# Performance work log

Measured on AMD Instinct MI355X. Metric: run time of the kernel, lower is better.

Reference implementation:

```python
import jax, jax.numpy as jnp
import numpy as np


def setup_inputs() -> dict:
    key = jax.random.key(0)
    ks = jax.random.split(key, 5)
    n, raw, d, h = 1024, 128, 128, 256
    s = lambda fan: 1.0 / np.sqrt(fan)
    return {
        "x": jax.random.normal(ks[0], (n, raw), jnp.float32),
        "W_enc": jax.random.normal(ks[1], (raw, d), jnp.float32) * s(raw),
        "b_enc": jnp.zeros((d,), jnp.float32),
        "W1": jax.random.normal(ks[2], (2 * d, h), jnp.float32) * s(2 * d),
        "b1": jnp.zeros((h,), jnp.float32),
        "W2": jax.random.normal(ks[3], (h, 1), jnp.float32) * s(h),
        "b2": jnp.zeros((1,), jnp.float32),
    }


def reference(x, W_enc, b_enc, W1, b1, W2, b2):
    # pathVAE.encode stand-in: linear projection to latent mean
    z = x @ W_enc + b_enc                      # [n, d]
    n, d = z.shape
    # Original builds feat[i, j] = concat(z[j], z[i]) of shape [n*n, 2d],
    # then Linear(2d->h). Split W1 so the quadratic concat is never built:
    # h[i, j] = z[j] @ W1[:d] + z[i] @ W1[d:] + b1
    A = z @ W1[:d]                             # acts on the "a" (j) half
    B = z @ W1[d:]                             # acts on the "b" (i) half
    hmat = A[None, :, :] + B[:, None, :] + b1  # [n, n, h]
    hmat = jax.nn.selu(hmat)
    o = hmat @ W2 + b2                         # [n, n, 1]
    o = jax.nn.hard_sigmoid(o)                 # relu6(x+3)/6, same as torch
    return o.reshape(n, n)
```

## Files before the change

kernel.cpp:

```cpp
#include <hip/hip_runtime.h>
#include <math.h>


#define LOG2E       1.4426950408889634f
#define SELU_AS     1.7580993408473766f
#define S_OVER_L2E  0.7282921587620419f

typedef float v2f __attribute__((ext_vector_type(2)));
typedef _Float16 v2h __attribute__((ext_vector_type(2)));
typedef unsigned int u32;

__global__ __launch_bounds__(256) void prep_kernel(
    const float* __restrict__ x, const float* __restrict__ W_enc,
    const float* __restrict__ b_enc, const float* __restrict__ W1,
    const float* __restrict__ b1, const float* __restrict__ W2,
    const float* __restrict__ b2, u32* __restrict__ PAa,
    u32* __restrict__ PAe, u32* __restrict__ PBb, u32* __restrict__ PBe,
    u32* __restrict__ W2m, u32* __restrict__ W2e, float* __restrict__ basep)
{
    __shared__ float zs[512];
    int t = threadIdx.x, b = blockIdx.x;
    if (b < 256) {
        int r0 = b << 2;
        int r = t >> 6;
        int dd = (t & 63) << 1;
        const float* xr = x + (size_t)(r0 + r) * 128;
        v2f z = { b_enc[dd], b_enc[dd + 1] };
#pragma unroll 8
        for (int dl = 0; dl < 128; ++dl) {
            float xv = xr[dl];
            v2f xx = { xv, xv };
            v2f wv = *(const v2f*)(W_enc + (size_t)dl * 128 + dd);
            z = __builtin_elementwise_fma(xx, wv, z);
        }
        zs[r * 128 + dd] = z.x;
        zs[r * 128 + dd + 1] = z.y;
        __syncthreads();

        int c = t;
        float b1c = b1[c];
        float accA0 = 0.f, accA1 = 0.f, accA2 = 0.f, accA3 = 0.f;
        float accB0 = b1c, accB1 = b1c, accB2 = b1c, accB3 = b1c;
        const float* w1a = W1 + c;
        const float* w1b = W1 + 128 * 256 + c;
#pragma unroll 4
        for (int dl = 0; dl < 128; ++dl) {
            float wa = w1a[(size_t)dl * 256];
            float wb = w1b[(size_t)dl * 256];
            float z0 = zs[dl], z1 = zs[128 + dl], z2 = zs[256 + dl], z3 = zs[384 + dl];
            accA0 = fmaf(z0, wa, accA0); accB0 = fmaf(z0, wb, accB0);
            accA1 = fmaf(z1, wa, accA1); accB1 = fmaf(z1, wb, accB1);
            accA2 = fmaf(z2, wa, accA2); accB2 = fmaf(z2, wb, accB2);
            accA3 = fmaf(z3, wa, accA3); accB3 = fmaf(z3, wb, accB3);
        }
        float ar[4] = { accA0 * LOG2E, accA1 * LOG2E, accA2 * LOG2E, accA3 * LOG2E };
        float br[4] = { accB0 * LOG2E, accB1 * LOG2E, accB2 * LOG2E, accB3 * LOG2E };
        u32 pa[4], pe[4], pb[4], pf[4];
        bool odd = (c & 1);
#pragma unroll
        for (int r2 = 0; r2 < 4; ++r2) {
            float er = __builtin_amdgcn_exp2f(ar[r2]);
            float fr = __builtin_amdgcn_exp2f(br[r2]);
            float aN = __shfl_xor(ar[r2], 1);
            float eN = __shfl_xor(er, 1);
            float bN = __shfl_xor(br[r2], 1);
            float fN = __shfl_xor(fr, 1);
            pa[r2] = __builtin_bit_cast(u32, __builtin_amdgcn_cvt_pkrtz(ar[r2], aN));
            pe[r2] = __builtin_bit_cast(u32, __builtin_amdgcn_cvt_pkrtz(er, eN));
            pb[r2] = __builtin_bit_cast(u32, __builtin_amdgcn_cvt_pkrtz(bN, br[r2]));
            pf[r2] = __builtin_bit_cast(u32, __builtin_amdgcn_cvt_pkrtz(fN, fr));
        }
        size_t o = (size_t)(c >> 1) * 1024 + r0;
        if (!odd) {
            *(uint4*)(PAa + o) = make_uint4(pa[0], pa[1], pa[2], pa[3]);
            *(uint4*)(PAe + o) = make_uint4(pe[0], pe[1], pe[2], pe[3]);
        } else {
            *(uint4*)(PBb + o) = make_uint4(pb[0], pb[1], pb[2], pb[3]);
            *(uint4*)(PBe + o) = make_uint4(pf[0], pf[1], pf[2], pf[3]);
        }
    } else {
        if (t < 128) {
            float w0 = W2[2 * t], w1 = W2[2 * t + 1];
            W2m[t] = __builtin_bit_cast(u32,
                __builtin_amdgcn_cvt_pkrtz(S_OVER_L2E * w0, S_OVER_L2E * w1));
            W2e[t] = __builtin_bit_cast(u32,
                __builtin_amdgcn_cvt_pkrtz(SELU_AS * w0, SELU_AS * w1));
        }
        if (t < 64) {
            float s = W2[t] + W2[t + 64] + W2[t + 128] + W2[t + 192];
#pragma unroll
            for (int o = 32; o > 0; o >>= 1) s += __shfl_down(s, o);
            if (t == 0) basep[0] = fmaf(-SELU_AS, s, b2[0]);
        }
    }
}

__global__ __launch_bounds__(256, 4) void pair_kernel(
    const u32* __restrict__ PAa, const u32* __restrict__ PAe,
    const u32* __restrict__ PBb, const u32* __restrict__ PBe,
    const u32* __restrict__ W2m, const u32* __restrict__ W2e,
    float* __restrict__ P)
{
    __shared__ __align__(16) u32 Aa[32 * 64];
    __shared__ __align__(16) u32 Ae[32 * 64];
    __shared__ __align__(16) u32 Bb[32 * 64];
    __shared__ __align__(16) u32 Be[32 * 64];

    int t = threadIdx.x;
    int bj64 = blockIdx.x << 6, bi64 = blockIdx.y << 6;
    int kc = blockIdx.z;
    int tj4 = (t & 15) << 2, ti4 = (t >> 4) << 2;

    float acc[4][4];
#pragma unroll
    for (int i = 0; i < 4; ++i)
#pragma unroll
        for (int j = 0; j < 4; ++j) acc[i][j] = 0.f;

    const v2h hzero = { (_Float16)0.f, (_Float16)0.f };
    const v2h hone  = { (_Float16)1.f, (_Float16)1.f };

#pragma unroll
    for (int p = 0; p < 2; ++p) {
        int q = (p << 8) + t;
        int k2l = q >> 4;
        int jq = (q & 15) << 2;
        size_t go = (size_t)((kc << 5) + k2l) * 1024;
        *(uint4*)&Aa[q << 2] = *(const uint4*)(PAa + go + bj64 + jq);
        *(uint4*)&Ae[q << 2] = *(const uint4*)(PAe + go + bj64 + jq);
        *(uint4*)&Bb[q << 2] = *(const uint4*)(PBb + go + bi64 + jq);
        *(uint4*)&Be[q << 2] = *(const uint4*)(PBe + go + bi64 + jq);
    }
    __syncthreads();

    const u32* Wm = W2m + (kc << 5);
    const u32* We = W2e + (kc << 5);
#pragma unroll 4
    for (int k2 = 0; k2 < 32; ++k2) {
        v2h w2m = __builtin_bit_cast(v2h, Wm[k2]);
        v2h w2e = __builtin_bit_cast(v2h, We[k2]);
        uint4 qa = *(const uint4*)&Aa[(k2 << 6) + tj4];
        uint4 qe = *(const uint4*)&Ae[(k2 << 6) + tj4];
        uint4 qb = *(const uint4*)&Bb[(k2 << 6) + ti4];
        uint4 qf = *(const uint4*)&Be[(k2 << 6) + ti4];
        v2h a[4] = { __builtin_bit_cast(v2h, qa.x), __builtin_bit_cast(v2h, qa.y),
                     __builtin_bit_cast(v2h, qa.z), __builtin_bit_cast(v2h, qa.w) };
        v2h e[4] = { __builtin_bit_cast(v2h, qe.x), __builtin_bit_cast(v2h, qe.y),
                     __builtin_bit_cast(v2h, qe.z), __builtin_bit_cast(v2h, qe.w) };
        v2h bb[4] = { __builtin_bit_cast(v2h, qb.x), __builtin_bit_cast(v2h, qb.y),
                      __builtin_bit_cast(v2h, qb.z), __builtin_bit_cast(v2h, qb.w) };
        v2h ff[4] = { __builtin_bit_cast(v2h, qf.x), __builtin_bit_cast(v2h, qf.y),
                      __builtin_bit_cast(v2h, qf.z), __builtin_bit_cast(v2h, qf.w) };
#pragma unroll
        for (int i = 0; i < 4; ++i) {
#pragma unroll
            for (int j = 0; j < 4; ++j) {
                v2h t2 = a[j] + bb[i];
                v2h p2 = e[j] * ff[i];
                v2h m2 = __builtin_elementwise_max(t2, hzero);
                v2h n2 = __builtin_elementwise_min(p2, hone);
                acc[i][j] = __builtin_amdgcn_fdot2(m2, w2m, acc[i][j], false);
                acc[i][j] = __builtin_amdgcn_fdot2(n2, w2e, acc[i][j], false);
            }
        }
    }

    float* Pc = P + ((size_t)kc << 20);
#pragma unroll
    for (int i = 0; i < 4; ++i) {
        float4 o;
        o.x = acc[i][0]; o.y = acc[i][1]; o.z = acc[i][2]; o.w = acc[i][3];
        *(float4*)(Pc + (size_t)(bi64 + ti4 + i) * 1024 + bj64 + tj4) = o;
    }
}

__global__ __launch_bounds__(256) void combine_kernel(
    const float* __restrict__ P, const float* __restrict__ basep,
    float* __restrict__ out)
{
    int idx = (blockIdx.x * 256 + threadIdx.x) << 2;
    float4 p0 = *(const float4*)(P + idx);
    float4 p1 = *(const float4*)(P + (1 << 20) + idx);
    float4 p2 = *(const float4*)(P + (2 << 20) + idx);
    float4 p3 = *(const float4*)(P + (3 << 20) + idx);
    float base = basep[0];
    float4 o;
    o.x = __saturatef((p0.x + p1.x + p2.x + p3.x + base) * (1.0f / 6.0f) + 0.5f);
    o.y = __saturatef((p0.y + p1.y + p2.y + p3.y + base) * (1.0f / 6.0f) + 0.5f);
    o.z = __saturatef((p0.z + p1.z + p2.z + p3.z + base) * (1.0f / 6.0f) + 0.5f);
    o.w = __saturatef((p0.w + p1.w + p2.w + p3.w + base) * (1.0f / 6.0f) + 0.5f);
    *(float4*)(out + idx) = o;
}

extern "C" void kernel_launch(void* const* d_in, const int* in_sizes, int n_in,
                              void* d_out, int out_size, void* d_ws, size_t ws_size,
                              hipStream_t stream) {
    const float* x     = (const float*)d_in[0];
    const float* W_enc = (const float*)d_in[1];
    const float* b_enc = (const float*)d_in[2];
    const float* W1    = (const float*)d_in[3];
    const float* b1    = (const float*)d_in[4];
    const float* W2    = (const float*)d_in[5];
    const float* b2    = (const float*)d_in[6];
    float* out = (float*)d_out;

    u32* ws = (u32*)d_ws;
    const int PLANE = 128 * 1024;
    u32* PAa = ws;
    u32* PAe = ws + PLANE;
    u32* PBb = ws + 2 * PLANE;
    u32* PBe = ws + 3 * PLANE;
    u32* W2m = ws + 4 * PLANE;
    u32* W2e = ws + 4 * PLANE + 128;
    float* basep = (float*)(ws + 4 * PLANE + 256);
    float* P = (float*)(ws + 4 * PLANE + 512);

    prep_kernel<<<257, 256, 0, stream>>>(x, W_enc, b_enc, W1, b1, W2, b2,
                                         PAa, PAe, PBb, PBe, W2m, W2e, basep);
    pair_kernel<<<dim3(16, 16, 4), 256, 0, stream>>>(PAa, PAe, PBb, PBe,
                                                     W2m, W2e, P);
    combine_kernel<<<1024, 256, 0, stream>>>(P, basep, out);
}
```

Baseline: 117.5 us.

## Fuse k-split partial reduction and combine into pair kernel via LDS

```diff
diff --git a/kernel.cpp b/kernel.cpp
--- a/kernel.cpp
+++ b/kernel.cpp
@@ -95,21 +95,25 @@
     }
 }
 
-__global__ __launch_bounds__(256, 4) void pair_kernel(
+__global__ __launch_bounds__(1024, 4) void pair_kernel(
     const u32* __restrict__ PAa, const u32* __restrict__ PAe,
     const u32* __restrict__ PBb, const u32* __restrict__ PBe,
     const u32* __restrict__ W2m, const u32* __restrict__ W2e,
-    float* __restrict__ P)
+    const float* __restrict__ basep, float* __restrict__ out)
 {
-    __shared__ __align__(16) u32 Aa[32 * 64];
-    __shared__ __align__(16) u32 Ae[32 * 64];
-    __shared__ __align__(16) u32 Bb[32 * 64];
-    __shared__ __align__(16) u32 Be[32 * 64];
+    __shared__ __align__(16) u32 S[16384];
 
     int t = threadIdx.x;
+    int q = t >> 8;
+    int tq = t & 255;
     int bj64 = blockIdx.x << 6, bi64 = blockIdx.y << 6;
-    int kc = blockIdx.z;
-    int tj4 = (t & 15) << 2, ti4 = (t >> 4) << 2;
+    int tj4 = (tq & 15) << 2, ti4 = (tq >> 4) << 2;
+
+    u32* Q  = S + (q << 12);
+    u32* Aa = Q;
+    u32* Ae = Q + 1024;
+    u32* Bb = Q + 2048;
+    u32* Be = Q + 3072;
 
     float acc[4][4];
 #pragma unroll
@@ -120,76 +124,87 @@
     const v2h hzero = { (_Float16)0.f, (_Float16)0.f };
     const v2h hone  = { (_Float16)1.f, (_Float16)1.f };
 
-#pragma unroll
-    for (int p = 0; p < 2; ++p) {
-        int q = (p << 8) + t;
-        int k2l = q >> 4;
-        int jq = (q & 15) << 2;
-        size_t go = (size_t)((kc << 5) + k2l) * 1024;
-        *(uint4*)&Aa[q << 2] = *(const uint4*)(PAa + go + bj64 + jq);
-        *(uint4*)&Ae[q << 2] = *(const uint4*)(PAe + go + bj64 + jq);
-        *(uint4*)&Bb[q << 2] = *(const uint4*)(PBb + go + bi64 + jq);
-        *(uint4*)&Be[q << 2] = *(const uint4*)(PBe + go + bi64 + jq);
-    }
+    int s_k2l = tq >> 4;
+    int s_jq  = (tq & 15) << 2;
+
+    for (int sc = 0; sc < 2; ++sc) {
+        int k2base = (q << 5) + (sc << 4);
+        if (sc) __syncthreads();
+        {
+            size_t go = (size_t)(k2base + s_k2l) * 1024;
+            *(uint4*)&Aa[tq << 2] = *(const uint4*)(PAa + go + bj64 + s_jq);
+            *(uint4*)&Ae[tq << 2] = *(const uint4*)(PAe + go + bj64 + s_jq);
+            *(uint4*)&Bb[tq << 2] = *(const uint4*)(PBb + go + bi64 + s_jq);
+            *(uint4*)&Be[tq << 2] = *(const uint4*)(PBe + go + bi64 + s_jq);
+        }
+        __syncthreads();
+
+        const u32* Wm = W2m + k2base;
+        const u32* We = W2e + k2base;
+#pragma unroll 4
+        for (int k2 = 0; k2 < 16; ++k2) {
+            v2h w2m = __builtin_bit_cast(v2h, Wm[k2]);
+            v2h w2e = __builtin_bit_cast(v2h, We[k2]);
+            uint4 qa = *(const uint4*)&Aa[(k2 << 6) + tj4];
+            uint4 qe = *(const uint4*)&Ae[(k2 << 6) + tj4];
+            uint4 qb = *(const uint4*)&Bb[(k2 << 6) + ti4];
+            uint4 qf = *(const uint4*)&Be[(k2 << 6) + ti4];
+            v2h a[4] = { __builtin_bit_cast(v2h, qa.x), __builtin_bit_cast(v2h, qa.y),
+                         __builtin_bit_cast(v2h, qa.z), __builtin_bit_cast(v2h, qa.w) };
+            v2h e[4] = { __builtin_bit_cast(v2h, qe.x), __builtin_bit_cast(v2h, qe.y),
+                         __builtin_bit_cast(v2h, qe.z), __builtin_bit_cast(v2h, qe.w) };
+            v2h bb[4] = { __builtin_bit_cast(v2h, qb.x), __builtin_bit_cast(v2h, qb.y),
+                          __builtin_bit_cast(v2h, qb.z), __builtin_bit_cast(v2h, qb.w) };
+            v2h ff[4] = { __builtin_bit_cast(v2h, qf.x), __builtin_bit_cast(v2h, qf.y),
+                          __builtin_bit_cast(v2h, qf.z), __builtin_bit_cast(v2h, qf.w) };
+#pragma unroll
+            for (int i = 0; i < 4; ++i) {
+#pragma unroll
+                for (int j = 0; j < 4; ++j) {
+                    v2h t2 = a[j] + bb[i];
+                    v2h p2 = e[j] * ff[i];
+                    v2h m2 = __builtin_elementwise_max(t2, hzero);
+                    v2h n2 = __builtin_elementwise_min(p2, hone);
+                    acc[i][j] = __builtin_amdgcn_fdot2(m2, w2m, acc[i][j], false);
+                    acc[i][j] = __builtin_amdgcn_fdot2(n2, w2e, acc[i][j], false);
+                }
+            }
+        }
+    }
+
     __syncthreads();
-
-    const u32* Wm = W2m + (kc << 5);
-    const u32* We = W2e + (kc << 5);
-#pragma unroll 4
-    for (int k2 = 0; k2 < 32; ++k2) {
-        v2h w2m = __builtin_bit_cast(v2h, Wm[k2]);
-        v2h w2e = __builtin_bit_cast(v2h, We[k2]);
-        uint4 qa = *(const uint4*)&Aa[(k2 << 6) + tj4];
-        uint4 qe = *(const uint4*)&Ae[(k2 << 6) + tj4];
-        uint4 qb = *(const uint4*)&Bb[(k2 << 6) + ti4];
-        uint4 qf = *(const uint4*)&Be[(k2 << 6) + ti4];
-        v2h a[4] = { __builtin_bit_cast(v2h, qa.x), __builtin_bit_cast(v2h, qa.y),
-                     __builtin_bit_cast(v2h, qa.z), __builtin_bit_cast(v2h, qa.w) };
-        v2h e[4] = { __builtin_bit_cast(v2h, qe.x), __builtin_bit_cast(v2h, qe.y),
-                     __builtin_bit_cast(v2h, qe.z), __builtin_bit_cast(v2h, qe.w) };
-        v2h bb[4] = { __builtin_bit_cast(v2h, qb.x), __builtin_bit_cast(v2h, qb.y),
-                      __builtin_bit_cast(v2h, qb.z), __builtin_bit_cast(v2h, qb.w) };
-        v2h ff[4] = { __builtin_bit_cast(v2h, qf.x), __builtin_bit_cast(v2h, qf.y),
-                      __builtin_bit_cast(v2h, qf.z), __builtin_bit_cast(v2h, qf.w) };
+    if (q != 0) {
+        float4* dst = (float4*)Q;
 #pragma unroll
         for (int i = 0; i < 4; ++i) {
-#pragma unroll
-            for (int j = 0; j < 4; ++j) {
-                v2h t2 = a[j] + bb[i];
-                v2h p2 = e[j] * ff[i];
-                v2h m2 = __builtin_elementwise_max(t2, hzero);
-                v2h n2 = __builtin_elementwise_min(p2, hone);
-                acc[i][j] = __builtin_amdgcn_fdot2(m2, w2m, acc[i][j], false);
-                acc[i][j] = __builtin_amdgcn_fdot2(n2, w2e, acc[i][j], false);
-            }
-        }
-    }
-
-    float* Pc = P + ((size_t)kc << 20);
-#pragma unroll
-    for (int i = 0; i < 4; ++i) {
-        float4 o;
-        o.x = acc[i][0]; o.y = acc[i][1]; o.z = acc[i][2]; o.w = acc[i][3];
-        *(float4*)(Pc + (size_t)(bi64 + ti4 + i) * 1024 + bj64 + tj4) = o;
-    }
-}
-
-__global__ __launch_bounds__(256) void combine_kernel(
-    const float* __restrict__ P, const float* __restrict__ basep,
-    float* __restrict__ out)
-{
-    int idx = (blockIdx.x * 256 + threadIdx.x) << 2;
-    float4 p0 = *(const float4*)(P + idx);
-    float4 p1 = *(const float4*)(P + (1 << 20) + idx);
-    float4 p2 = *(const float4*)(P + (2 << 20) + idx);
-    float4 p3 = *(const float4*)(P + (3 << 20) + idx);
-    float base = basep[0];
-    float4 o;
-    o.x = __saturatef((p0.x + p1.x + p2.x + p3.x + base) * (1.0f / 6.0f) + 0.5f);
-    o.y = __saturatef((p0.y + p1.y + p2.y + p3.y + base) * (1.0f / 6.0f) + 0.5f);
-    o.z = __saturatef((p0.z + p1.z + p2.z + p3.z + base) * (1.0f / 6.0f) + 0.5f);
-    o.w = __saturatef((p0.w + p1.w + p2.w + p3.w + base) * (1.0f / 6.0f) + 0.5f);
-    *(float4*)(out + idx) = o;
+            float4 v;
+            v.x = acc[i][0]; v.y = acc[i][1]; v.z = acc[i][2]; v.w = acc[i][3];
+            dst[(tq << 2) + i] = v;
+        }
+    }
+    __syncthreads();
+    if (q == 0) {
+        float base = basep[0];
+        const float4* Q1 = (const float4*)(S + 4096);
+        const float4* Q2 = (const float4*)(S + 8192);
+        const float4* Q3 = (const float4*)(S + 12288);
+#pragma unroll
+        for (int i = 0; i < 4; ++i) {
+            float4 p1 = Q1[(tq << 2) + i];
+            float4 p2 = Q2[(tq << 2) + i];
+            float4 p3 = Q3[(tq << 2) + i];
+            float v0 = acc[i][0] + p1.x + p2.x + p3.x + base;
+            float v1 = acc[i][1] + p1.y + p2.y + p3.y + base;
+            float v2 = acc[i][2] + p1.z + p2.z + p3.z + base;
+            float v3 = acc[i][3] + p1.w + p2.w + p3.w + base;
+            float4 o;
+            o.x = __saturatef(v0 * (1.0f / 6.0f) + 0.5f);
+            o.y = __saturatef(v1 * (1.0f / 6.0f) + 0.5f);
+            o.z = __saturatef(v2 * (1.0f / 6.0f) + 0.5f);
+            o.w = __saturatef(v3 * (1.0f / 6.0f) + 0.5f);
+            *(float4*)(out + (size_t)(bi64 + ti4 + i) * 1024 + bj64 + tj4) = o;
+        }
+    }
 }
 
 extern "C" void kernel_launch(void* const* d_in, const int* in_sizes, int n_in,
@@ -213,11 +228,9 @@
     u32* W2m = ws + 4 * PLANE;
     u32* W2e = ws + 4 * PLANE + 128;
     float* basep = (float*)(ws + 4 * PLANE + 256);
-    float* P = (float*)(ws + 4 * PLANE + 512);
 
     prep_kernel<<<257, 256, 0, stream>>>(x, W_enc, b_enc, W1, b1, W2, b2,
                                          PAa, PAe, PBb, PBe, W2m, W2e, basep);
-    pair_kernel<<<dim3(16, 16, 4), 256, 0, stream>>>(PAa, PAe, PBb, PBe,
-                                                     W2m, W2e, P);
-    combine_kernel<<<1024, 256, 0, stream>>>(P, basep, out);
+    pair_kernel<<<dim3(16, 16), 1024, 0, stream>>>(PAa, PAe, PBb, PBe,
+                                                   W2m, W2e, basep, out);
 }
```

After: 112.2 us. 1.05x faster.
